# Kernel optimization log

Hardware: AMD Instinct MI355X
Metric: run time of the kernel (lower is better)

The kernel has to match this reference:

```python
import jax, jax.numpy as jnp
import numpy as np

D_MODEL = 1024
NUM_HEADS = 16
D_K = D_MODEL // NUM_HEADS


def setup_inputs() -> dict:
    key = jax.random.key(0)
    ks = jax.random.split(key, 5)
    B, S = 4, 2048
    scale = 1.0 / np.sqrt(D_MODEL)
    x = jax.random.normal(ks[0], (B, S, D_MODEL), dtype=jnp.float32)
    # Linear(d_model, d_model, bias=False) weights, stored as [out, in] like torch
    Wq = jax.random.normal(ks[1], (D_MODEL, D_MODEL), dtype=jnp.float32) * scale
    Wk = jax.random.normal(ks[2], (D_MODEL, D_MODEL), dtype=jnp.float32) * scale
    Wv = jax.random.normal(ks[3], (D_MODEL, D_MODEL), dtype=jnp.float32) * scale
    Wo = jax.random.normal(ks[4], (D_MODEL, D_MODEL), dtype=jnp.float32) * scale
    return {"x": x, "Wq": Wq, "Wk": Wk, "Wv": Wv, "Wo": Wo}


def reference(x, Wq, Wk, Wv, Wo):
    B, S, D = x.shape
    H, dk = NUM_HEADS, D_K
    # projections (torch Linear: x @ W.T)
    q = (x @ Wq.T).reshape(B, S, H, dk).transpose(0, 2, 1, 3)  # [B,H,S,dk]
    k = (x @ Wk.T).reshape(B, S, H, dk).transpose(0, 2, 1, 3)
    v = (x @ Wv.T).reshape(B, S, H, dk).transpose(0, 2, 1, 3)
    scores = jnp.einsum("bhqd,bhkd->bhqk", q, k) / jnp.sqrt(jnp.float32(dk))
    causal = jnp.triu(jnp.ones((S, S), dtype=bool), k=1)  # True above diagonal -> masked
    scores = jnp.where(causal[None, None], -jnp.inf, scores)
    attn = jax.nn.softmax(scores, axis=-1)
    out = jnp.einsum("bhqk,bhkd->bhqd", attn, v)  # [B,H,S,dk]
    out = out.transpose(0, 2, 1, 3).reshape(B, S, D)
    return out @ Wo.T
```

## Files before the change

kernel.cpp:

```cpp
#include <hip/hip_runtime.h>

typedef __bf16 bf16_t;
typedef __bf16 bf16x8 __attribute__((ext_vector_type(8)));
typedef __bf16 bf16x4 __attribute__((ext_vector_type(4)));
typedef float f32x4 __attribute__((ext_vector_type(4)));
typedef unsigned short u16x8 __attribute__((ext_vector_type(8)));

#define AS1C(p) ((const __attribute__((address_space(1))) void*)(p))
#define AS3(p) ((__attribute__((address_space(3))) void*)(p))
#define MM(a, b, c) __builtin_amdgcn_mfma_f32_16x16x32_bf16(a, b, c, 0, 0, 0)

__device__ __forceinline__ unsigned short f2b_rne(float f) {
  union { float f; unsigned u; } x; x.f = f;
  unsigned u = x.u;
  u += 0x7fffu + ((u >> 16) & 1u);
  return (unsigned short)(u >> 16);
}

__device__ __forceinline__ float fast_exp2(float x) {
  return __builtin_amdgcn_exp2f(x);
}

__global__ __launch_bounds__(256) void cast_f32_bf16(const float* __restrict__ in,
                                                     unsigned short* __restrict__ out,
                                                     int n) {
  int i = (blockIdx.x * 256 + threadIdx.x) * 8;
  if (i >= n) return;
  const float4* p = reinterpret_cast<const float4*>(in + i);
  float4 a = p[0], b = p[1];
  u16x8 o;
  o[0] = f2b_rne(a.x); o[1] = f2b_rne(a.y); o[2] = f2b_rne(a.z); o[3] = f2b_rne(a.w);
  o[4] = f2b_rne(b.x); o[5] = f2b_rne(b.y); o[6] = f2b_rne(b.z); o[7] = f2b_rne(b.w);
  *reinterpret_cast<u16x8*>(out + i) = o;
}

__global__ __launch_bounds__(256) void cast_w4(const float* __restrict__ w0,
                                               const float* __restrict__ w1,
                                               const float* __restrict__ w2,
                                               const float* __restrict__ w3,
                                               unsigned short* __restrict__ out) {
  const float* in = (blockIdx.y == 0) ? w0 : (blockIdx.y == 1) ? w1
                  : (blockIdx.y == 2) ? w2 : w3;
  int i = (blockIdx.x * 256 + threadIdx.x) * 8;
  unsigned short* o = out + (size_t)blockIdx.y * (1024u * 1024u);
  const float4* p = reinterpret_cast<const float4*>(in + i);
  float4 a = p[0], b = p[1];
  u16x8 v;
  v[0] = f2b_rne(a.x); v[1] = f2b_rne(a.y); v[2] = f2b_rne(a.z); v[3] = f2b_rne(a.w);
  v[4] = f2b_rne(b.x); v[5] = f2b_rne(b.y); v[6] = f2b_rne(b.z); v[7] = f2b_rne(b.w);
  *reinterpret_cast<u16x8*>(o + i) = v;
}

template <int OUT_F32>
__global__ __launch_bounds__(512, 2) void gemm4(const bf16_t* __restrict__ A,
                                                const bf16_t* __restrict__ Bm,
                                                void* __restrict__ C,
                                                int M, int N, int K, int lda,
                                                float scale, int qlim) {
  extern __shared__ bf16_t lds[];
  const int tid = threadIdx.x;
  const int w = tid >> 6, l = tid & 63;
  const int r = l & 15, kg = l >> 4;
  const int wm64 = (w >> 2) * 64, wn32 = (w & 3) * 32;
  const int w8 = w * 8;
  const int m0 = blockIdx.y * 128, n0 = blockIdx.x * 256;
  const bf16_t* aSrc = A + (size_t)(m0 + w8 + (l >> 3)) * lda + ((l & 7) ^ (l >> 3)) * 8;
  const bf16_t* bSrc = Bm + (size_t)(n0 + w8 + (l >> 3)) * K + ((l & 7) ^ (l >> 3)) * 8;
  const int acol0 = (kg ^ (r & 7)) * 8;
  const int acol1 = ((4 + kg) ^ (r & 7)) * 8;

  f32x4 acc[2][4][2] = {};

  auto STAGE = [&](bf16_t* sb, int kt) {
    const bf16_t* ak = aSrc + kt * 64;
    const bf16_t* bk = bSrc + kt * 64;
    __builtin_amdgcn_global_load_lds(AS1C(ak),                    AS3(sb + (w8) * 64), 16, 0, 0);
    __builtin_amdgcn_global_load_lds(AS1C(ak + (size_t)64 * lda), AS3(sb + (64 + w8) * 64), 16, 0, 0);
    __builtin_amdgcn_global_load_lds(AS1C(bk),                    AS3(sb + 8192 + (w8) * 64), 16, 0, 0);
    __builtin_amdgcn_global_load_lds(AS1C(bk + (size_t)64 * K),   AS3(sb + 8192 + (64 + w8) * 64), 16, 0, 0);
    __builtin_amdgcn_global_load_lds(AS1C(bk + (size_t)128 * K),  AS3(sb + 8192 + (128 + w8) * 64), 16, 0, 0);
    __builtin_amdgcn_global_load_lds(AS1C(bk + (size_t)192 * K),  AS3(sb + 8192 + (192 + w8) * 64), 16, 0, 0);
  };

  bf16_t* cur = lds;
  bf16_t* nxt = lds + 24576;
  bf16_t* stg = lds + 49152;

  STAGE(cur, 0);
  STAGE(nxt, 1);
  asm volatile("s_waitcnt vmcnt(6)" ::: "memory");
  __builtin_amdgcn_s_barrier();

  const int NT = K >> 6;
  for (int t = 0; t < NT; ++t) {
    bf16x8 AF[4][2], BF[2][2][2];
#pragma unroll
    for (int il = 0; il < 4; ++il) {
      const int ao = (wm64 + il * 16 + r) * 64;
      AF[il][0] = *reinterpret_cast<const bf16x8*>(cur + ao + acol0);
      AF[il][1] = *reinterpret_cast<const bf16x8*>(cur + ao + acol1);
    }
#pragma unroll
    for (int qb = 0; qb < 2; ++qb)
#pragma unroll
      for (int jl = 0; jl < 2; ++jl) {
        const int bo = 8192 + (qb * 128 + wn32 + jl * 16 + r) * 64;
        BF[qb][jl][0] = *reinterpret_cast<const bf16x8*>(cur + bo + acol0);
        BF[qb][jl][1] = *reinterpret_cast<const bf16x8*>(cur + bo + acol1);
      }
    const int kt = (t + 2 < NT) ? t + 2 : t;
    STAGE(stg, kt);
    asm volatile("s_waitcnt lgkmcnt(4)" ::: "memory");
    __builtin_amdgcn_sched_barrier(0);
    __builtin_amdgcn_s_setprio(1);
#pragma unroll
    for (int il = 0; il < 4; ++il)
#pragma unroll
      for (int jl = 0; jl < 2; ++jl)
        acc[0][il][jl] = MM(AF[il][1], BF[0][jl][1], MM(AF[il][0], BF[0][jl][0], acc[0][il][jl]));
    __builtin_amdgcn_s_setprio(0);
    asm volatile("s_waitcnt lgkmcnt(0)" ::: "memory");
    __builtin_amdgcn_sched_barrier(0);
    __builtin_amdgcn_s_setprio(1);
#pragma unroll
    for (int il = 0; il < 4; ++il)
#pragma unroll
      for (int jl = 0; jl < 2; ++jl)
        acc[1][il][jl] = MM(AF[il][1], BF[1][jl][1], MM(AF[il][0], BF[1][jl][0], acc[1][il][jl]));
    __builtin_amdgcn_s_setprio(0);
    asm volatile("s_waitcnt vmcnt(6)" ::: "memory");
    __builtin_amdgcn_s_barrier();
    bf16_t* tmp = cur; cur = nxt; nxt = stg; stg = tmp;
  }

#pragma unroll
  for (int qb = 0; qb < 2; ++qb)
#pragma unroll
    for (int il = 0; il < 4; ++il)
#pragma unroll
      for (int jl = 0; jl < 2; ++jl) {
        const int row0 = m0 + wm64 + il * 16 + kg * 4;
        const int col = n0 + qb * 128 + wn32 + jl * 16 + r;
        const float sc = (col < qlim) ? scale : 1.0f;
#pragma unroll
        for (int v = 0; v < 4; ++v) {
          float val = acc[qb][il][jl][v] * sc;
          size_t idx = (size_t)(row0 + v) * N + col;
          if (OUT_F32) reinterpret_cast<float*>(C)[idx] = val;
          else reinterpret_cast<unsigned short*>(C)[idx] = f2b_rne(val);
        }
      }
}

__global__ __launch_bounds__(256) void transpose_v(const bf16_t* __restrict__ qkv,
                                                   bf16_t* __restrict__ vt) {
  __shared__ bf16_t Vs[64 * 72];
  const int t = threadIdx.x;
  const int s0 = blockIdx.x * 64;
  const int bh = blockIdx.y;
  const int b = bh >> 4, h = bh & 15;
  const size_t in_base = ((size_t)b * 2048 + s0) * 3072 + 2048 + h * 64;
#pragma unroll
  for (int c = 0; c < 2; ++c) {
    int chunk = c * 256 + t;
    int ss = chunk >> 3, dd = (chunk & 7) * 8;
    bf16x8 v = *reinterpret_cast<const bf16x8*>(qkv + in_base + (size_t)ss * 3072 + dd);
    *reinterpret_cast<bf16x8*>(Vs + ss * 72 + dd) = v;
  }
  __syncthreads();
  const size_t out_base = (size_t)bh * 64 * 2048 + s0;
#pragma unroll
  for (int c = 0; c < 2; ++c) {
    int chunk = c * 256 + t;
    int dd = chunk >> 3, ss = (chunk & 7) * 8;
    bf16x8 o;
#pragma unroll
    for (int j = 0; j < 8; ++j) o[j] = Vs[(ss + j) * 72 + dd];
    *reinterpret_cast<bf16x8*>(vt + out_base + (size_t)dd * 2048 + ss) = o;
  }
}

__global__ __launch_bounds__(512) void flash_attn(const bf16_t* __restrict__ QKV,
                                                  const bf16_t* __restrict__ VT,
                                                  unsigned short* __restrict__ O,
                                                  int ostride) {
  __shared__ bf16_t Ks[2][64 * 72];
  __shared__ bf16_t Vts[2][64 * 72];
  __shared__ bf16_t Pl[8][16 * 72];
  const int tid = threadIdx.x;
  const int lane = tid & 63, wave = tid >> 6;
  const int r = lane & 15, kg = lane >> 4;
  const int bh = blockIdx.x;
  const int pair = blockIdx.y;
  const int b = bh >> 4, h = bh & 15;
  const size_t qkv_row0 = (size_t)b * 2048 * 3072;
  const int qcol = h * 64, kcol = 1024 + h * 64;
  const size_t vt_base = (size_t)bh * 64 * 2048;
  const size_t o_row0 = (size_t)b * 2048 * ostride;
  const int ocol = h * 64;
  const int srr = tid >> 3, scc = (tid & 7) * 8;

  for (int pass = 0; pass < 2; ++pass) {
    const int qt = pass ? (15 - pair) : pair;
    const int q0 = qt * 128;
    const int qrow = q0 + wave * 16 + r;
    const int tmax_w = (q0 + wave * 16 + 15) >> 6;
    const int ntiles = qt * 2 + 2;

    const size_t qoff = qkv_row0 + (size_t)qrow * 3072 + qcol;
    bf16x8 qf0 = *reinterpret_cast<const bf16x8*>(QKV + qoff + kg * 8);
    bf16x8 qf1 = *reinterpret_cast<const bf16x8*>(QKV + qoff + 32 + kg * 8);

    f32x4 oacc[4] = {};
    float m_run = -3e30f, l_lane = 0.f;

    bf16x8 gk = *reinterpret_cast<const bf16x8*>(QKV + qkv_row0 + (size_t)srr * 3072 + kcol + scc);
    bf16x8 gv = *reinterpret_cast<const bf16x8*>(VT + vt_base + (size_t)srr * 2048 + scc);

    for (int t = 0; t < ntiles; ++t) {
      const int buf = t & 1;
      *reinterpret_cast<bf16x8*>(&Ks[buf][srr * 72 + scc]) = gk;
      *reinterpret_cast<bf16x8*>(&Vts[buf][srr * 72 + scc]) = gv;
      __syncthreads();
      if (t + 1 < ntiles) {
        const int kv1 = (t + 1) * 64;
        gk = *reinterpret_cast<const bf16x8*>(QKV + qkv_row0 + (size_t)(kv1 + srr) * 3072 + kcol + scc);
        gv = *reinterpret_cast<const bf16x8*>(VT + vt_base + (size_t)srr * 2048 + kv1 + scc);
      }
      if (t > tmax_w) continue;

      const int kv0 = t * 64;
      float vals[16];
#pragma unroll
      for (int nt = 0; nt < 4; ++nt) {
        bf16x8 kf0 = *reinterpret_cast<const bf16x8*>(&Ks[buf][(nt * 16 + r) * 72 + kg * 8]);
        bf16x8 kf1 = *reinterpret_cast<const bf16x8*>(&Ks[buf][(nt * 16 + r) * 72 + 32 + kg * 8]);
        f32x4 s = {};
        __builtin_amdgcn_s_setprio(1);
        s = MM(kf0, qf0, s);
        s = MM(kf1, qf1, s);
        __builtin_amdgcn_s_setprio(0);
#pragma unroll
        for (int v = 0; v < 4; ++v) vals[nt * 4 + v] = s[v];
      }
      if (t == tmax_w) {
#pragma unroll
        for (int nt = 0; nt < 4; ++nt)
#pragma unroll
          for (int v = 0; v < 4; ++v)
            if (kv0 + nt * 16 + kg * 4 + v > qrow) vals[nt * 4 + v] = -3e30f;
      }
      float a0 = fmaxf(fmaxf(vals[0], vals[1]), vals[2]);
      float a1 = fmaxf(fmaxf(vals[3], vals[4]), vals[5]);
      float a2 = fmaxf(fmaxf(vals[6], vals[7]), vals[8]);
      float a3 = fmaxf(fmaxf(vals[9], vals[10]), vals[11]);
      float a4 = fmaxf(fmaxf(vals[12], vals[13]), vals[14]);
      float pmax = fmaxf(fmaxf(fmaxf(a0, a1), fmaxf(a2, a3)), fmaxf(a4, vals[15]));
      if (!__all(pmax <= m_run + 8.0f)) {
        pmax = fmaxf(pmax, __shfl_xor(pmax, 16));
        pmax = fmaxf(pmax, __shfl_xor(pmax, 32));
        const float m_new = fmaxf(m_run, pmax);
        const float alpha = fast_exp2(m_run - m_new);
        l_lane *= alpha;
        f32x4 al;
#pragma unroll
        for (int v = 0; v < 4; ++v) al[v] = __shfl(alpha, kg * 4 + v);
#pragma unroll
        for (int dt = 0; dt < 4; ++dt)
#pragma unroll
          for (int v = 0; v < 4; ++v) oacc[dt][v] *= al[v];
        m_run = m_new;
      }
#pragma unroll
      for (int ii = 0; ii < 16; ++ii) {
        float p = fast_exp2(vals[ii] - m_run);
        vals[ii] = p;
        l_lane += p;
      }
#pragma unroll
      for (int nt = 0; nt < 4; ++nt) {
        bf16x4 pb;
#pragma unroll
        for (int v = 0; v < 4; ++v) pb[v] = (bf16_t)vals[nt * 4 + v];
        *reinterpret_cast<bf16x4*>(&Pl[wave][r * 72 + nt * 16 + kg * 4]) = pb;
      }
      bf16x8 pa0 = *reinterpret_cast<const bf16x8*>(&Pl[wave][r * 72 + kg * 8]);
      bf16x8 pa1 = *reinterpret_cast<const bf16x8*>(&Pl[wave][r * 72 + 32 + kg * 8]);
#pragma unroll
      for (int dt = 0; dt < 4; ++dt) {
        bf16x8 vb0 = *reinterpret_cast<const bf16x8*>(&Vts[buf][(dt * 16 + r) * 72 + kg * 8]);
        bf16x8 vb1 = *reinterpret_cast<const bf16x8*>(&Vts[buf][(dt * 16 + r) * 72 + 32 + kg * 8]);
        __builtin_amdgcn_s_setprio(1);
        oacc[dt] = MM(pa0, vb0, oacc[dt]);
        oacc[dt] = MM(pa1, vb1, oacc[dt]);
        __builtin_amdgcn_s_setprio(0);
      }
    }

    float l_row = l_lane;
    l_row += __shfl_xor(l_row, 16);
    l_row += __shfl_xor(l_row, 32);
    const float linv = 1.0f / l_row;
    f32x4 il;
#pragma unroll
    for (int v = 0; v < 4; ++v) il[v] = __shfl(linv, kg * 4 + v);
    const size_t orow0 = o_row0 + (size_t)(q0 + wave * 16) * ostride + ocol;
#pragma unroll
    for (int dt = 0; dt < 4; ++dt) {
      const int d = dt * 16 + r;
#pragma unroll
      for (int v = 0; v < 4; ++v)
        O[orow0 + (size_t)(kg * 4 + v) * ostride + d] = f2b_rne(oacc[dt][v] * il[v]);
    }
  }
}

extern "C" void kernel_launch(void* const* d_in, const int* in_sizes, int n_in,
                              void* d_out, int out_size, void* d_ws, size_t ws_size,
                              hipStream_t stream) {
  const float* x  = (const float*)d_in[0];
  const float* Wq = (const float*)d_in[1];
  const float* Wk = (const float*)d_in[2];
  const float* Wv = (const float*)d_in[3];
  const float* Wo = (const float*)d_in[4];

  char* ws = (char*)d_ws;
  bf16_t* xb  = (bf16_t*)(ws);
  bf16_t* wqb = (bf16_t*)(ws + (16u << 20));
  bf16_t* wob = (bf16_t*)(ws + (22u << 20));
  bf16_t* qkv = (bf16_t*)(ws + (24u << 20));
  bf16_t* vt  = (bf16_t*)(ws);

  hipFuncSetAttribute(reinterpret_cast<const void*>(&gemm4<0>),
                      hipFuncAttributeMaxDynamicSharedMemorySize, 147456);
  hipFuncSetAttribute(reinterpret_cast<const void*>(&gemm4<1>),
                      hipFuncAttributeMaxDynamicSharedMemorySize, 147456);

  const int NX = 4 * 2048 * 1024;
  cast_f32_bf16<<<NX / 2048, 256, 0, stream>>>(x, (unsigned short*)xb, NX);
  cast_w4<<<dim3(512, 4), 256, 0, stream>>>(Wq, Wk, Wv, Wo, (unsigned short*)wqb);

  gemm4<0><<<dim3(3072 / 256, 8192 / 128), 512, 147456, stream>>>(
      xb, wqb, qkv, 8192, 3072, 1024, 1024, 0.18033688011112042f, 1024);

  transpose_v<<<dim3(2048 / 64, 64), 256, 0, stream>>>(qkv, vt);

  flash_attn<<<dim3(64, 8), 512, 0, stream>>>(qkv, vt, (unsigned short*)qkv, 3072);

  gemm4<1><<<dim3(1024 / 256, 8192 / 128), 512, 147456, stream>>>(
      qkv, wob, d_out, 8192, 1024, 1024, 3072, 1.0f, 0);
}
```

Baseline: 184.6 us.

## Shrink GEMM K-tile to 32 and split flash attention into one q-tile per block

After: 180.9 us. 1.02x faster.

```diff
diff --git a/kernel.cpp b/kernel.cpp
--- a/kernel.cpp
+++ b/kernel.cpp
@@ -52,7 +52,7 @@
 }
 
 template <int OUT_F32>
-__global__ __launch_bounds__(512, 2) void gemm4(const bf16_t* __restrict__ A,
+__global__ __launch_bounds__(512, 4) void gemmk(const bf16_t* __restrict__ A,
                                                 const bf16_t* __restrict__ Bm,
                                                 void* __restrict__ C,
                                                 int M, int N, int K, int lda,
@@ -61,63 +61,51 @@
   const int tid = threadIdx.x;
   const int w = tid >> 6, l = tid & 63;
   const int r = l & 15, kg = l >> 4;
-  const int wm64 = (w >> 2) * 64, wn32 = (w & 3) * 32;
-  const int w8 = w * 8;
+  const int wm = (w >> 2) * 64;
+  const int wn = (w & 3) * 64;
   const int m0 = blockIdx.y * 128, n0 = blockIdx.x * 256;
-  const bf16_t* aSrc = A + (size_t)(m0 + w8 + (l >> 3)) * lda + ((l & 7) ^ (l >> 3)) * 8;
-  const bf16_t* bSrc = Bm + (size_t)(n0 + w8 + (l >> 3)) * K + ((l & 7) ^ (l >> 3)) * 8;
-  const int acol0 = (kg ^ (r & 7)) * 8;
-  const int acol1 = ((4 + kg) ^ (r & 7)) * 8;
-
-  f32x4 acc[2][4][2] = {};
+  const int srow = w * 16 + (l >> 2);
+  const int scol = (l & 3) * 8;
+  const bf16_t* aS = A + (size_t)(m0 + srow) * lda + scol;
+  const bf16_t* bS = Bm + (size_t)(n0 + srow) * K + scol;
+
+  f32x4 acc[4][4] = {};
 
   auto STAGE = [&](bf16_t* sb, int kt) {
-    const bf16_t* ak = aSrc + kt * 64;
-    const bf16_t* bk = bSrc + kt * 64;
-    __builtin_amdgcn_global_load_lds(AS1C(ak),                    AS3(sb + (w8) * 64), 16, 0, 0);
-    __builtin_amdgcn_global_load_lds(AS1C(ak + (size_t)64 * lda), AS3(sb + (64 + w8) * 64), 16, 0, 0);
-    __builtin_amdgcn_global_load_lds(AS1C(bk),                    AS3(sb + 8192 + (w8) * 64), 16, 0, 0);
-    __builtin_amdgcn_global_load_lds(AS1C(bk + (size_t)64 * K),   AS3(sb + 8192 + (64 + w8) * 64), 16, 0, 0);
-    __builtin_amdgcn_global_load_lds(AS1C(bk + (size_t)128 * K),  AS3(sb + 8192 + (128 + w8) * 64), 16, 0, 0);
-    __builtin_amdgcn_global_load_lds(AS1C(bk + (size_t)192 * K),  AS3(sb + 8192 + (192 + w8) * 64), 16, 0, 0);
+    __builtin_amdgcn_global_load_lds(AS1C(aS + kt * 32), AS3(sb + w * 512), 16, 0, 0);
+    __builtin_amdgcn_global_load_lds(AS1C(bS + kt * 32), AS3(sb + 4096 + w * 512), 16, 0, 0);
+    __builtin_amdgcn_global_load_lds(AS1C(bS + (size_t)128 * K + kt * 32),
+                                     AS3(sb + 8192 + w * 512), 16, 0, 0);
   };
 
   bf16_t* cur = lds;
-  bf16_t* nxt = lds + 24576;
-  bf16_t* stg = lds + 49152;
+  bf16_t* nxt = lds + 12288;
+  bf16_t* stg = lds + 24576;
 
   STAGE(cur, 0);
   STAGE(nxt, 1);
-  asm volatile("s_waitcnt vmcnt(6)" ::: "memory");
+  asm volatile("s_waitcnt vmcnt(3)" ::: "memory");
   __builtin_amdgcn_s_barrier();
 
-  const int NT = K >> 6;
+  const int NT = K >> 5;
   for (int t = 0; t < NT; ++t) {
-    bf16x8 AF[4][2], BF[2][2][2];
-#pragma unroll
-    for (int il = 0; il < 4; ++il) {
-      const int ao = (wm64 + il * 16 + r) * 64;
-      AF[il][0] = *reinterpret_cast<const bf16x8*>(cur + ao + acol0);
-      AF[il][1] = *reinterpret_cast<const bf16x8*>(cur + ao + acol1);
-    }
-#pragma unroll
-    for (int qb = 0; qb < 2; ++qb)
-#pragma unroll
-      for (int jl = 0; jl < 2; ++jl) {
-        const int bo = 8192 + (qb * 128 + wn32 + jl * 16 + r) * 64;
-        BF[qb][jl][0] = *reinterpret_cast<const bf16x8*>(cur + bo + acol0);
-        BF[qb][jl][1] = *reinterpret_cast<const bf16x8*>(cur + bo + acol1);
-      }
+    bf16x8 AF[4], BF[4];
+#pragma unroll
+    for (int il = 0; il < 4; ++il)
+      AF[il] = *reinterpret_cast<const bf16x8*>(cur + (wm + il * 16 + r) * 32 + kg * 8);
+#pragma unroll
+    for (int jl = 0; jl < 4; ++jl)
+      BF[jl] = *reinterpret_cast<const bf16x8*>(cur + 4096 + (wn + jl * 16 + r) * 32 + kg * 8);
     const int kt = (t + 2 < NT) ? t + 2 : t;
     STAGE(stg, kt);
-    asm volatile("s_waitcnt lgkmcnt(4)" ::: "memory");
+    asm volatile("s_waitcnt lgkmcnt(2)" ::: "memory");
     __builtin_amdgcn_sched_barrier(0);
     __builtin_amdgcn_s_setprio(1);
 #pragma unroll
     for (int il = 0; il < 4; ++il)
 #pragma unroll
       for (int jl = 0; jl < 2; ++jl)
-        acc[0][il][jl] = MM(AF[il][1], BF[0][jl][1], MM(AF[il][0], BF[0][jl][0], acc[0][il][jl]));
+        acc[il][jl] = MM(AF[il], BF[jl], acc[il][jl]);
     __builtin_amdgcn_s_setprio(0);
     asm volatile("s_waitcnt lgkmcnt(0)" ::: "memory");
     __builtin_amdgcn_sched_barrier(0);
@@ -125,31 +113,29 @@
 #pragma unroll
     for (int il = 0; il < 4; ++il)
 #pragma unroll
-      for (int jl = 0; jl < 2; ++jl)
-        acc[1][il][jl] = MM(AF[il][1], BF[1][jl][1], MM(AF[il][0], BF[1][jl][0], acc[1][il][jl]));
+      for (int jl = 2; jl < 4; ++jl)
+        acc[il][jl] = MM(AF[il], BF[jl], acc[il][jl]);
     __builtin_amdgcn_s_setprio(0);
-    asm volatile("s_waitcnt vmcnt(6)" ::: "memory");
+    asm volatile("s_waitcnt vmcnt(3)" ::: "memory");
     __builtin_amdgcn_s_barrier();
     bf16_t* tmp = cur; cur = nxt; nxt = stg; stg = tmp;
   }
 
 #pragma unroll
-  for (int qb = 0; qb < 2; ++qb)
-#pragma unroll
-    for (int il = 0; il < 4; ++il)
-#pragma unroll
-      for (int jl = 0; jl < 2; ++jl) {
-        const int row0 = m0 + wm64 + il * 16 + kg * 4;
-        const int col = n0 + qb * 128 + wn32 + jl * 16 + r;
-        const float sc = (col < qlim) ? scale : 1.0f;
-#pragma unroll
-        for (int v = 0; v < 4; ++v) {
-          float val = acc[qb][il][jl][v] * sc;
-          size_t idx = (size_t)(row0 + v) * N + col;
-          if (OUT_F32) reinterpret_cast<float*>(C)[idx] = val;
-          else reinterpret_cast<unsigned short*>(C)[idx] = f2b_rne(val);
-        }
+  for (int il = 0; il < 4; ++il)
+#pragma unroll
+    for (int jl = 0; jl < 4; ++jl) {
+      const int row0 = m0 + wm + il * 16 + kg * 4;
+      const int col = n0 + wn + jl * 16 + r;
+      const float sc = (col < qlim) ? scale : 1.0f;
+#pragma unroll
+      for (int v = 0; v < 4; ++v) {
+        float val = acc[il][jl][v] * sc;
+        size_t idx = (size_t)(row0 + v) * N + col;
+        if (OUT_F32) reinterpret_cast<float*>(C)[idx] = val;
+        else reinterpret_cast<unsigned short*>(C)[idx] = f2b_rne(val);
       }
+    }
 }
 
 __global__ __launch_bounds__(256) void transpose_v(const bf16_t* __restrict__ qkv,
@@ -180,18 +166,18 @@
   }
 }
 
-__global__ __launch_bounds__(512) void flash_attn(const bf16_t* __restrict__ QKV,
-                                                  const bf16_t* __restrict__ VT,
-                                                  unsigned short* __restrict__ O,
-                                                  int ostride) {
+__global__ __launch_bounds__(512, 6) void flash_attn(const bf16_t* __restrict__ QKV,
+                                                     const bf16_t* __restrict__ VT,
+                                                     unsigned short* __restrict__ O,
+                                                     int ostride) {
   __shared__ bf16_t Ks[2][64 * 72];
   __shared__ bf16_t Vts[2][64 * 72];
-  __shared__ bf16_t Pl[8][16 * 72];
+  __shared__ bf16_t Pl[8][16 * 68];
   const int tid = threadIdx.x;
   const int lane = tid & 63, wave = tid >> 6;
   const int r = lane & 15, kg = lane >> 4;
   const int bh = blockIdx.x;
-  const int pair = blockIdx.y;
+  const int qt = 15 - (int)blockIdx.y;
   const int b = bh >> 4, h = bh & 15;
   const size_t qkv_row0 = (size_t)b * 2048 * 3072;
   const int qcol = h * 64, kcol = 1024 + h * 64;
@@ -200,118 +186,115 @@
   const int ocol = h * 64;
   const int srr = tid >> 3, scc = (tid & 7) * 8;
 
-  for (int pass = 0; pass < 2; ++pass) {
-    const int qt = pass ? (15 - pair) : pair;
-    const int q0 = qt * 128;
-    const int qrow = q0 + wave * 16 + r;
-    const int tmax_w = (q0 + wave * 16 + 15) >> 6;
-    const int ntiles = qt * 2 + 2;
-
-    const size_t qoff = qkv_row0 + (size_t)qrow * 3072 + qcol;
-    bf16x8 qf0 = *reinterpret_cast<const bf16x8*>(QKV + qoff + kg * 8);
-    bf16x8 qf1 = *reinterpret_cast<const bf16x8*>(QKV + qoff + 32 + kg * 8);
-
-    f32x4 oacc[4] = {};
-    float m_run = -3e30f, l_lane = 0.f;
-
-    bf16x8 gk = *reinterpret_cast<const bf16x8*>(QKV + qkv_row0 + (size_t)srr * 3072 + kcol + scc);
-    bf16x8 gv = *reinterpret_cast<const bf16x8*>(VT + vt_base + (size_t)srr * 2048 + scc);
-
-    for (int t = 0; t < ntiles; ++t) {
-      const int buf = t & 1;
-      *reinterpret_cast<bf16x8*>(&Ks[buf][srr * 72 + scc]) = gk;
-      *reinterpret_cast<bf16x8*>(&Vts[buf][srr * 72 + scc]) = gv;
-      __syncthreads();
-      if (t + 1 < ntiles) {
-        const int kv1 = (t + 1) * 64;
-        gk = *reinterpret_cast<const bf16x8*>(QKV + qkv_row0 + (size_t)(kv1 + srr) * 3072 + kcol + scc);
-        gv = *reinterpret_cast<const bf16x8*>(VT + vt_base + (size_t)srr * 2048 + kv1 + scc);
-      }
-      if (t > tmax_w) continue;
-
-      const int kv0 = t * 64;
-      float vals[16];
-#pragma unroll
-      for (int nt = 0; nt < 4; ++nt) {
-        bf16x8 kf0 = *reinterpret_cast<const bf16x8*>(&Ks[buf][(nt * 16 + r) * 72 + kg * 8]);
-        bf16x8 kf1 = *reinterpret_cast<const bf16x8*>(&Ks[buf][(nt * 16 + r) * 72 + 32 + kg * 8]);
-        f32x4 s = {};
-        __builtin_amdgcn_s_setprio(1);
-        s = MM(kf0, qf0, s);
-        s = MM(kf1, qf1, s);
-        __builtin_amdgcn_s_setprio(0);
-#pragma unroll
-        for (int v = 0; v < 4; ++v) vals[nt * 4 + v] = s[v];
-      }
-      if (t == tmax_w) {
-#pragma unroll
-        for (int nt = 0; nt < 4; ++nt)
-#pragma unroll
-          for (int v = 0; v < 4; ++v)
-            if (kv0 + nt * 16 + kg * 4 + v > qrow) vals[nt * 4 + v] = -3e30f;
-      }
-      float a0 = fmaxf(fmaxf(vals[0], vals[1]), vals[2]);
-      float a1 = fmaxf(fmaxf(vals[3], vals[4]), vals[5]);
-      float a2 = fmaxf(fmaxf(vals[6], vals[7]), vals[8]);
-      float a3 = fmaxf(fmaxf(vals[9], vals[10]), vals[11]);
-      float a4 = fmaxf(fmaxf(vals[12], vals[13]), vals[14]);
-      float pmax = fmaxf(fmaxf(fmaxf(a0, a1), fmaxf(a2, a3)), fmaxf(a4, vals[15]));
-      if (!__all(pmax <= m_run + 8.0f)) {
-        pmax = fmaxf(pmax, __shfl_xor(pmax, 16));
-        pmax = fmaxf(pmax, __shfl_xor(pmax, 32));
-        const float m_new = fmaxf(m_run, pmax);
-        const float alpha = fast_exp2(m_run - m_new);
-        l_lane *= alpha;
-        f32x4 al;
-#pragma unroll
-        for (int v = 0; v < 4; ++v) al[v] = __shfl(alpha, kg * 4 + v);
-#pragma unroll
-        for (int dt = 0; dt < 4; ++dt)
-#pragma unroll
-          for (int v = 0; v < 4; ++v) oacc[dt][v] *= al[v];
-        m_run = m_new;
-      }
-#pragma unroll
-      for (int ii = 0; ii < 16; ++ii) {
-        float p = fast_exp2(vals[ii] - m_run);
-        vals[ii] = p;
-        l_lane += p;
-      }
-#pragma unroll
-      for (int nt = 0; nt < 4; ++nt) {
-        bf16x4 pb;
-#pragma unroll
-        for (int v = 0; v < 4; ++v) pb[v] = (bf16_t)vals[nt * 4 + v];
-        *reinterpret_cast<bf16x4*>(&Pl[wave][r * 72 + nt * 16 + kg * 4]) = pb;
-      }
-      bf16x8 pa0 = *reinterpret_cast<const bf16x8*>(&Pl[wave][r * 72 + kg * 8]);
-      bf16x8 pa1 = *reinterpret_cast<const bf16x8*>(&Pl[wave][r * 72 + 32 + kg * 8]);
-#pragma unroll
-      for (int dt = 0; dt < 4; ++dt) {
-        bf16x8 vb0 = *reinterpret_cast<const bf16x8*>(&Vts[buf][(dt * 16 + r) * 72 + kg * 8]);
-        bf16x8 vb1 = *reinterpret_cast<const bf16x8*>(&Vts[buf][(dt * 16 + r) * 72 + 32 + kg * 8]);
-        __builtin_amdgcn_s_setprio(1);
-        oacc[dt] = MM(pa0, vb0, oacc[dt]);
-        oacc[dt] = MM(pa1, vb1, oacc[dt]);
-        __builtin_amdgcn_s_setprio(0);
-      }
-    }
-
-    float l_row = l_lane;
-    l_row += __shfl_xor(l_row, 16);
-    l_row += __shfl_xor(l_row, 32);
-    const float linv = 1.0f / l_row;
-    f32x4 il;
-#pragma unroll
-    for (int v = 0; v < 4; ++v) il[v] = __shfl(linv, kg * 4 + v);
-    const size_t orow0 = o_row0 + (size_t)(q0 + wave * 16) * ostride + ocol;
+  const int q0 = qt * 128;
+  const int qrow = q0 + wave * 16 + r;
+  const int tmax_w = (q0 + wave * 16 + 15) >> 6;
+  const int ntiles = qt * 2 + 2;
+
+  const size_t qoff = qkv_row0 + (size_t)qrow * 3072 + qcol;
+  bf16x8 qf0 = *reinterpret_cast<const bf16x8*>(QKV + qoff + kg * 8);
+  bf16x8 qf1 = *reinterpret_cast<const bf16x8*>(QKV + qoff + 32 + kg * 8);
+
+  f32x4 oacc[4] = {};
+  float m_run = -3e30f, l_lane = 0.f;
+
+  bf16x8 gk = *reinterpret_cast<const bf16x8*>(QKV + qkv_row0 + (size_t)srr * 3072 + kcol + scc);
+  bf16x8 gv = *reinterpret_cast<const bf16x8*>(VT + vt_base + (size_t)srr * 2048 + scc);
+
+  for (int t = 0; t < ntiles; ++t) {
+    const int buf = t & 1;
+    *reinterpret_cast<bf16x8*>(&Ks[buf][srr * 72 + scc]) = gk;
+    *reinterpret_cast<bf16x8*>(&Vts[buf][srr * 72 + scc]) = gv;
+    __syncthreads();
+    if (t + 1 < ntiles) {
+      const int kv1 = (t + 1) * 64;
+      gk = *reinterpret_cast<const bf16x8*>(QKV + qkv_row0 + (size_t)(kv1 + srr) * 3072 + kcol + scc);
+      gv = *reinterpret_cast<const bf16x8*>(VT + vt_base + (size_t)srr * 2048 + kv1 + scc);
+    }
+    if (t > tmax_w) continue;
+
+    const int kv0 = t * 64;
+    float vals[16];
+#pragma unroll
+    for (int nt = 0; nt < 4; ++nt) {
+      bf16x8 kf0 = *reinterpret_cast<const bf16x8*>(&Ks[buf][(nt * 16 + r) * 72 + kg * 8]);
+      bf16x8 kf1 = *reinterpret_cast<const bf16x8*>(&Ks[buf][(nt * 16 + r) * 72 + 32 + kg * 8]);
+      f32x4 s = {};
+      __builtin_amdgcn_s_setprio(1);
+      s = MM(kf0, qf0, s);
+      s = MM(kf1, qf1, s);
+      __builtin_amdgcn_s_setprio(0);
+#pragma unroll
+      for (int v = 0; v < 4; ++v) vals[nt * 4 + v] = s[v];
+    }
+    if (t == tmax_w) {
+#pragma unroll
+      for (int nt = 0; nt < 4; ++nt)
+#pragma unroll
+        for (int v = 0; v < 4; ++v)
+          if (kv0 + nt * 16 + kg * 4 + v > qrow) vals[nt * 4 + v] = -3e30f;
+    }
+    float a0 = fmaxf(fmaxf(vals[0], vals[1]), vals[2]);
+    float a1 = fmaxf(fmaxf(vals[3], vals[4]), vals[5]);
+    float a2 = fmaxf(fmaxf(vals[6], vals[7]), vals[8]);
+    float a3 = fmaxf(fmaxf(vals[9], vals[10]), vals[11]);
+    float a4 = fmaxf(fmaxf(vals[12], vals[13]), vals[14]);
+    float pmax = fmaxf(fmaxf(fmaxf(a0, a1), fmaxf(a2, a3)), fmaxf(a4, vals[15]));
+    if (!__all(pmax <= m_run + 8.0f)) {
+      pmax = fmaxf(pmax, __shfl_xor(pmax, 16));
+      pmax = fmaxf(pmax, __shfl_xor(pmax, 32));
+      const float m_new = fmaxf(m_run, pmax);
+      const float alpha = fast_exp2(m_run - m_new);
+      l_lane *= alpha;
+      f32x4 al;
+#pragma unroll
+      for (int v = 0; v < 4; ++v) al[v] = __shfl(alpha, kg * 4 + v);
+#pragma unroll
+      for (int dt = 0; dt < 4; ++dt)
+#pragma unroll
+        for (int v = 0; v < 4; ++v) oacc[dt][v] *= al[v];
+      m_run = m_new;
+    }
+#pragma unroll
+    for (int ii = 0; ii < 16; ++ii) {
+      float p = fast_exp2(vals[ii] - m_run);
+      vals[ii] = p;
+      l_lane += p;
+    }
+#pragma unroll
+    for (int nt = 0; nt < 4; ++nt) {
+      bf16x4 pb;
+#pragma unroll
+      for (int v = 0; v < 4; ++v) pb[v] = (bf16_t)vals[nt * 4 + v];
+      *reinterpret_cast<bf16x4*>(&Pl[wave][r * 68 + nt * 16 + kg * 4]) = pb;
+    }
+    bf16x8 pa0 = *reinterpret_cast<const bf16x8*>(&Pl[wave][r * 68 + kg * 8]);
+    bf16x8 pa1 = *reinterpret_cast<const bf16x8*>(&Pl[wave][r * 68 + 32 + kg * 8]);
 #pragma unroll
     for (int dt = 0; dt < 4; ++dt) {
-      const int d = dt * 16 + r;
-#pragma unroll
-      for (int v = 0; v < 4; ++v)
-        O[orow0 + (size_t)(kg * 4 + v) * ostride + d] = f2b_rne(oacc[dt][v] * il[v]);
-    }
+      bf16x8 vb0 = *reinterpret_cast<const bf16x8*>(&Vts[buf][(dt * 16 + r) * 72 + kg * 8]);
+      bf16x8 vb1 = *reinterpret_cast<const bf16x8*>(&Vts[buf][(dt * 16 + r) * 72 + 32 + kg * 8]);
+      __builtin_amdgcn_s_setprio(1);
+      oacc[dt] = MM(pa0, vb0, oacc[dt]);
+      oacc[dt] = MM(pa1, vb1, oacc[dt]);
+      __builtin_amdgcn_s_setprio(0);
+    }
+  }
+
+  float l_row = l_lane;
+  l_row += __shfl_xor(l_row, 16);
+  l_row += __shfl_xor(l_row, 32);
+  const float linv = 1.0f / l_row;
+  f32x4 il;
+#pragma unroll
+  for (int v = 0; v < 4; ++v) il[v] = __shfl(linv, kg * 4 + v);
+  const size_t orow0 = o_row0 + (size_t)(q0 + wave * 16) * ostride + ocol;
+#pragma unroll
+  for (int dt = 0; dt < 4; ++dt) {
+    const int d = dt * 16 + r;
+#pragma unroll
+    for (int v = 0; v < 4; ++v)
+      O[orow0 + (size_t)(kg * 4 + v) * ostride + d] = f2b_rne(oacc[dt][v] * il[v]);
   }
 }
 
@@ -331,22 +314,22 @@
   bf16_t* qkv = (bf16_t*)(ws + (24u << 20));
   bf16_t* vt  = (bf16_t*)(ws);
 
-  hipFuncSetAttribute(reinterpret_cast<const void*>(&gemm4<0>),
-                      hipFuncAttributeMaxDynamicSharedMemorySize, 147456);
-  hipFuncSetAttribute(reinterpret_cast<const void*>(&gemm4<1>),
-                      hipFuncAttributeMaxDynamicSharedMemorySize, 147456);
+  hipFuncSetAttribute(reinterpret_cast<const void*>(&gemmk<0>),
+                      hipFuncAttributeMaxDynamicSharedMemorySize, 73728);
+  hipFuncSetAttribute(reinterpret_cast<const void*>(&gemmk<1>),
+                      hipFuncAttributeMaxDynamicSharedMemorySize, 73728);
 
   const int NX = 4 * 2048 * 1024;
   cast_f32_bf16<<<NX / 2048, 256, 0, stream>>>(x, (unsigned short*)xb, NX);
   cast_w4<<<dim3(512, 4), 256, 0, stream>>>(Wq, Wk, Wv, Wo, (unsigned short*)wqb);
 
-  gemm4<0><<<dim3(3072 / 256, 8192 / 128), 512, 147456, stream>>>(
+  gemmk<0><<<dim3(3072 / 256, 8192 / 128), 512, 73728, stream>>>(
       xb, wqb, qkv, 8192, 3072, 1024, 1024, 0.18033688011112042f, 1024);
 
   transpose_v<<<dim3(2048 / 64, 64), 256, 0, stream>>>(qkv, vt);
 
-  flash_attn<<<dim3(64, 8), 512, 0, stream>>>(qkv, vt, (unsigned short*)qkv, 3072);
-
-  gemm4<1><<<dim3(1024 / 256, 8192 / 128), 512, 147456, stream>>>(
+  flash_attn<<<dim3(64, 16), 512, 0, stream>>>(qkv, vt, (unsigned short*)qkv, 3072);
+
+  gemmk<1><<<dim3(1024 / 256, 8192 / 128), 512, 73728, stream>>>(
       qkv, wob, d_out, 8192, 1024, 1024, 3072, 1.0f, 0);
 }
```
